# Kernel optimization log

Hardware: AMD Instinct MI355X
Metric: run time of the kernel (lower is better)

## Reference

```python
import jax, jax.numpy as jnp
import numpy as np

B, N_NODES, T_IN = 512, 32, 12
HID, HEADS, OUT_CH, DEG = 64, 8, 9, 8


def setup_inputs() -> dict:
    key = jax.random.key(0)
    ks = jax.random.split(key, 26)
    rn = lambda k, s, sc=0.1: (jax.random.normal(k, s, jnp.float32) * sc)
    E = B * N_NODES * DEG
    src = jax.random.randint(ks[0], (E,), 0, N_NODES, jnp.int32)
    dst = jax.random.randint(ks[1], (E,), 0, N_NODES, jnp.int32)
    off = jnp.repeat(jnp.arange(B, dtype=jnp.int32) * N_NODES, N_NODES * DEG)
    edge_index = jnp.stack([src + off, dst + off])  # block-diagonal batched graph
    x = jax.random.normal(ks[2], (B, N_NODES, T_IN), jnp.float32)
    return {
        "x": x,
        "edge_index": edge_index,
        # gat1: in=T_IN -> HEADS*HID, concat
        "W1": rn(ks[3], (T_IN, HEADS * HID)),
        "a_src1": rn(ks[4], (HEADS, HID)),
        "a_dst1": rn(ks[5], (HEADS, HID)),
        "b1": rn(ks[6], (HEADS * HID,), 0.01),
        # gat2: in=HEADS*HID -> HID, heads=1, mean (concat=False)
        "W2": rn(ks[7], (HEADS * HID, HID), 0.05),
        "a_src2": rn(ks[8], (1, HID)),
        "a_dst2": rn(ks[9], (1, HID)),
        "b2": rn(ks[10], (HID,), 0.01),
        "gamma": jnp.ones((HID,), jnp.float32),
        "beta": jnp.zeros((HID,), jnp.float32),
        # gru1: input_size=N_NODES(=32), hidden=HID
        "Wi1": rn(ks[11], (3 * HID, N_NODES)),
        "Wh1": rn(ks[12], (3 * HID, HID)),
        "bi1": rn(ks[13], (3 * HID,), 0.01),
        "bh1": rn(ks[14], (3 * HID,), 0.01),
        # gru2: input_size=HID, hidden=HID
        "Wi2": rn(ks[15], (3 * HID, HID)),
        "Wh2": rn(ks[16], (3 * HID, HID)),
        "bi2": rn(ks[17], (3 * HID,), 0.01),
        "bh2": rn(ks[18], (3 * HID,), 0.01),
        "Wf": rn(ks[19], (OUT_CH, HID)),
        "bf": rn(ks[20], (OUT_CH,), 0.01),
    }


def _gat_layer(x, src, dst, W, a_s, a_d, b, concat):
    # PyG GATConv (eval mode, self-loops already appended by caller)
    Nn = x.shape[0]
    heads, hc = a_s.shape
    h = (x @ W).reshape(Nn, heads, hc)                 # [N, H, C]
    es = jnp.sum(h * a_s, axis=-1)                     # [N, H]
    ed = jnp.sum(h * a_d, axis=-1)
    e = jax.nn.leaky_relu(es[src] + ed[dst], 0.2)      # [E, H]
    m = jax.ops.segment_max(e, dst, num_segments=Nn)
    p = jnp.exp(e - m[dst])
    s = jax.ops.segment_sum(p, dst, num_segments=Nn)
    alpha = p / (s[dst] + 1e-16)                       # per-dst softmax
    out = jax.ops.segment_sum(h[src] * alpha[:, :, None], dst, num_segments=Nn)
    out = out.reshape(Nn, heads * hc) if concat else out.mean(axis=1)
    return out + b


def _gru(x, Wi, Wh, bi, bh):
    # torch.nn.GRU (batch_first) single layer; x: [B, T, F]
    H = Wh.shape[1]
    xi = x @ Wi.T + bi                                 # [B, T, 3H]
    def step(h, xt):
        gh = h @ Wh.T + bh
        r = jax.nn.sigmoid(xt[:, :H] + gh[:, :H])
        z = jax.nn.sigmoid(xt[:, H:2 * H] + gh[:, H:2 * H])
        n = jnp.tanh(xt[:, 2 * H:] + r * gh[:, 2 * H:])
        hn = (1.0 - z) * n + z * h
        return hn, hn
    h0 = jnp.zeros((x.shape[0], H), x.dtype)
    _, ys = jax.lax.scan(step, h0, jnp.swapaxes(xi, 0, 1))
    return jnp.swapaxes(ys, 0, 1)


def reference(x, edge_index, W1, a_src1, a_dst1, b1, W2, a_src2, a_dst2, b2,
              gamma, beta, Wi1, Wh1, bi1, bh1, Wi2, Wh2, bi2, bh2, Wf, bf):
    Bsz, Nn_, T = x.shape
    Nn = Bsz * Nn_
    xf = x.reshape(Nn, T)                              # dropout is identity in eval
    sl = jnp.arange(Nn, dtype=edge_index.dtype)        # PyG add_self_loops=True
    src = jnp.concatenate([edge_index[0], sl])
    dst = jnp.concatenate([edge_index[1], sl])
    h = jax.nn.elu(_gat_layer(xf, src, dst, W1, a_src1, a_dst1, b1, True))
    h = jax.nn.elu(_gat_layer(h, src, dst, W2, a_src2, a_dst2, b2, False))
    mu = h.mean(-1, keepdims=True)
    var = ((h - mu) ** 2).mean(-1, keepdims=True)
    h = (h - mu) / jnp.sqrt(var + 1e-5) * gamma + beta
    seq = h.reshape(Bsz, Nn_, -1).transpose(0, 2, 1)   # [B, HID(seq), N_NODES(feat)]
    g = _gru(seq, Wi1, Wh1, bi1, bh1)
    g = _gru(g, Wi2, Wh2, bi2, bh2)
    return g[:, -1, :] @ Wf.T + bf                     # [B, OUT_CH]
```

## Files before the change

### kernel.cpp

```cpp
#include <hip/hip_runtime.h>
#include <hip/hip_bf16.h>
#include <stdint.h>

#define BATCH 512
#define NN 32
#define T_IN 12
#define HID 64
#define HEADS 8
#define OUT_CH 9
#define EPB (NN*8)
#define ETOT (EPB+NN)
#define F1 (HEADS*HID)

using u16 = unsigned short;
using u32 = unsigned int;
typedef _Float16 f16;
typedef _Float16 f16x2 __attribute__((ext_vector_type(2)));
typedef u32 v4u __attribute__((ext_vector_type(4)));
typedef float v4f __attribute__((ext_vector_type(4)));

__device__ __forceinline__ float bf2f(u16 u){ return __uint_as_float(((u32)u)<<16); }
__device__ __forceinline__ u16 f2bf(float f){
    u32 x = __float_as_uint(f);
    u32 r = (x + 0x7FFFu + ((x>>16)&1u))>>16;
    return (u16)r;
}
__device__ __forceinline__ u32 packf16(float a, float b){
    f16x2 p; p.x=(f16)a; p.y=(f16)b; return __builtin_bit_cast(u32,p);
}
__device__ __forceinline__ u16 f2h16(float a){ f16 h=(f16)a; return __builtin_bit_cast(u16,h); }
__device__ __forceinline__ float lof(u32 w){ return (float)__builtin_bit_cast(f16x2,w).x; }
__device__ __forceinline__ float hif(u32 w){ return (float)__builtin_bit_cast(f16x2,w).y; }
__device__ __forceinline__ float dot2(u32 a, u32 b, float c){
#if __has_builtin(__builtin_amdgcn_fdot2)
    return __builtin_amdgcn_fdot2(__builtin_bit_cast(f16x2,a), __builtin_bit_cast(f16x2,b), c, false);
#else
    return fmaf(lof(a),lof(b), fmaf(hif(a),hif(b), c));
#endif
}
__device__ __forceinline__ float elu1(float x){ return x > 0.f ? x : (__expf(x)-1.f); }
__device__ __forceinline__ float sigm(float x){ return 1.f/(1.f+__expf(-x)); }
__device__ __forceinline__ float tanh_(float x){ return 1.f - 2.f/(__expf(2.f*x)+1.f); }
__device__ __forceinline__ u32 fenc(float v){
    u32 b=__float_as_uint(v);
    return (b&0x80000000u) ? ~b : (b|0x80000000u);
}
__device__ __forceinline__ float fdec(u32 k){
    return __uint_as_float((k&0x80000000u) ? (k&0x7FFFFFFFu) : ~k);
}

#define DOT4(acc,A,W) do{ acc=dot2(A.x,W.x,acc); acc=dot2(A.y,W.y,acc); \
                          acc=dot2(A.z,W.z,acc); acc=dot2(A.w,W.w,acc); }while(0)

struct CvtDesc {
    const void* src[16];
    void*       dst[16];
    int         n[16];
};

__global__ __launch_bounds__(256) void k_setup(
    const u32* __restrict__ xw, CvtDesc d,
    const void* __restrict__ W2src, u16* __restrict__ W2i,
    const void* __restrict__ Wi1, const void* __restrict__ Wh1,
    const void* __restrict__ Wi2, const void* __restrict__ Wh2,
    u32* __restrict__ wpk, int* __restrict__ flag)
{
    __shared__ int cnt;
    if(threadIdx.x==0) cnt=0;
    __syncthreads();
    int c=0;
    for(int i=threadIdx.x;i<4096;i+=256){
        u32 w=xw[i];
        if(w & 0x7FFFFFFFu){
            u32 el=(w>>7)&0xFFu;
            if(el>=0x90u) c++;
        }
    }
    atomicAdd(&cnt,c);
    __syncthreads();
    const int f = (cnt>256) ? 1 : 0;
    if(blockIdx.x==0 && threadIdx.x==0) *flag=f;

    const int bk=blockIdx.x;
    if(bk<128){
        int seg=bk>>3, sub=bk&7;
        const void* s=d.src[seg];
        float* o=(float*)d.dst[seg];
        int n=d.n[seg];
        for(int i=sub*256+threadIdx.x;i<n;i+=2048)
            o[i] = f ? ((const float*)s)[i] : bf2f(((const u16*)s)[i]);
    } else if(bk<256){
        int i=(bk-128)*256+threadIdx.x;
        int k=i>>6, j=i&63;
        float v = f? ((const float*)W2src)[i] : bf2f(((const u16*)W2src)[i]);
        W2i[ (((size_t)(k>>3)*64 + j)<<3) + (k&7) ] = f2h16(v);
    } else {
        int w=(bk-256)*256+threadIdx.x;
        int m=w/6144;
        int rem=w-m*6144;
        int row=rem>>5, kw=rem&31;
        const void* s=(m==0)?Wi1:(m==1)?Wh1:(m==2)?Wi2:Wh2;
        int K=(m==0)?32:64;
        int k0=2*kw, k1=k0+1;
        float v0=0.f, v1=0.f;
        if(k0<K) v0 = f? ((const float*)s)[row*K+k0] : bf2f(((const u16*)s)[row*K+k0]);
        if(k1<K) v1 = f? ((const float*)s)[row*K+k1] : bf2f(((const u16*)s)[row*K+k1]);
        wpk[w]=packf16(v0,v1);
    }
}

__global__ __launch_bounds__(512,4) void k_fused(
    const float* __restrict__ x, const int* __restrict__ ei,
    const float* __restrict__ W1, const float* __restrict__ a_s, const float* __restrict__ a_d,
    const float* __restrict__ b1,
    const uint4* __restrict__ W2i, const float* __restrict__ a_s2, const float* __restrict__ a_d2,
    const float* __restrict__ b2, const float* __restrict__ gam, const float* __restrict__ bet,
    const u32* __restrict__ wpk,
    const float* __restrict__ bi1, const float* __restrict__ bh1,
    const float* __restrict__ bi2, const float* __restrict__ bh2,
    const float* __restrict__ Wf, const float* __restrict__ bfv,
    void* __restrict__ outp, const int* __restrict__ flag)
{
    const int b = blockIdx.x, t = threadIdx.x;

    __shared__ __align__(16) float s_x[NN][12];
    __shared__ __align__(16) u16 s_h[NN][520];
    __shared__ __align__(16) u32 s_aspk[HEADS*32], s_adpk[HEADS*32];
    __shared__ float s_es[NN][HEADS], s_ed[NN][HEADS];
    __shared__ unsigned char s_src[ETOT], s_dst[ETOT];
    __shared__ float s_al[HEADS][ETOT];
    __shared__ u32 s_mx[NN*HEADS];
    __shared__ float s_sm[NN*HEADS], s_inv[NN*HEADS];
    __shared__ int s_cnt[NN], s_off[NN], s_fil[NN];
    __shared__ short s_lst[ETOT];
    __shared__ float s_h2[NN][HID];
    __shared__ __align__(16) u32 s_x1[64*16];
    __shared__ __align__(16) u32 s_g1[2][32];
    __shared__ __align__(16) u32 s_g2[2][32];
    __shared__ float s_h2f[64];

    for(int i=t;i<NN*T_IN;i+=512) s_x[i/12][i%12] = x[b*NN*T_IN + i];
    if(t<256){
        s_aspk[t]=packf16(a_s[2*t],a_s[2*t+1]);
        s_adpk[t]=packf16(a_d[2*t],a_d[2*t+1]);
        s_mx[t]=0u; s_sm[t]=0.f;
    }
    if(t<EPB){
        s_src[t] = (unsigned char)(ei[b*EPB+t] - b*NN);
        s_dst[t] = (unsigned char)(ei[(size_t)BATCH*EPB + b*EPB+t] - b*NN);
    }
    if(t<NN){ s_src[EPB+t]=s_dst[EPB+t]=(unsigned char)t; s_cnt[t]=0; s_fil[t]=0; }
    v4f Wc0,Wc1,Wc2;
    Wc0.x=W1[0*F1+t]; Wc0.y=W1[1*F1+t]; Wc0.z=W1[2*F1+t]; Wc0.w=W1[3*F1+t];
    Wc1.x=W1[4*F1+t]; Wc1.y=W1[5*F1+t]; Wc1.z=W1[6*F1+t]; Wc1.w=W1[7*F1+t];
    Wc2.x=W1[8*F1+t]; Wc2.y=W1[9*F1+t]; Wc2.z=W1[10*F1+t]; Wc2.w=W1[11*F1+t];
    __syncthreads();

    for(int n=0;n<NN;n++){
        const float4* xp=(const float4*)s_x[n];
        float4 xa=xp[0], xb=xp[1], xc=xp[2];
        float A=0.f;
        A=fmaf(xa.x,Wc0.x,A); A=fmaf(xa.y,Wc0.y,A); A=fmaf(xa.z,Wc0.z,A); A=fmaf(xa.w,Wc0.w,A);
        A=fmaf(xb.x,Wc1.x,A); A=fmaf(xb.y,Wc1.y,A); A=fmaf(xb.z,Wc1.z,A); A=fmaf(xb.w,Wc1.w,A);
        A=fmaf(xc.x,Wc2.x,A); A=fmaf(xc.y,Wc2.y,A); A=fmaf(xc.z,Wc2.z,A); A=fmaf(xc.w,Wc2.w,A);
        s_h[n][t]=f2h16(A);
    }
    for(int e=t;e<ETOT;e+=512) atomicAdd(&s_cnt[s_dst[e]],1);
    __syncthreads();

    if(t<256){
        int n=t&31, hd=t>>5;
        const v4u* hp=(const v4u*)((const u16*)s_h[n] + hd*64);
        v4u h0=hp[0],h1=hp[1],h2=hp[2],h3=hp[3],h4=hp[4],h5=hp[5],h6=hp[6],h7=hp[7];
        const v4u* ap=(const v4u*)&s_aspk[hd*32];
        const v4u* dp=(const v4u*)&s_adpk[hd*32];
        float e1=0.f,e2=0.f;
        { v4u w=ap[0]; DOT4(e1,h0,w); w=ap[1]; DOT4(e1,h1,w); w=ap[2]; DOT4(e1,h2,w); w=ap[3]; DOT4(e1,h3,w);
          w=ap[4]; DOT4(e1,h4,w); w=ap[5]; DOT4(e1,h5,w); w=ap[6]; DOT4(e1,h6,w); w=ap[7]; DOT4(e1,h7,w); }
        { v4u w=dp[0]; DOT4(e2,h0,w); w=dp[1]; DOT4(e2,h1,w); w=dp[2]; DOT4(e2,h2,w); w=dp[3]; DOT4(e2,h3,w);
          w=dp[4]; DOT4(e2,h4,w); w=dp[5]; DOT4(e2,h5,w); w=dp[6]; DOT4(e2,h6,w); w=dp[7]; DOT4(e2,h7,w); }
        s_es[n][hd]=e1; s_ed[n][hd]=e2;
    }
    if(t==0){ int o=0; for(int i=0;i<NN;i++){ s_off[i]=o; o+=s_cnt[i]; } }
    __syncthreads();

    for(int e=t;e<ETOT;e+=512){
        int d=s_dst[e]; int p=atomicAdd(&s_fil[d],1); s_lst[s_off[d]+p]=(short)e;
    }
    for(int i=t;i<ETOT*HEADS;i+=512){
        int hd=i/ETOT, e=i-hd*ETOT;
        int sr=s_src[e], d=s_dst[e];
        float v = s_es[sr][hd]+s_ed[d][hd];
        v = v>0.f? v : 0.2f*v;
        s_al[hd][e]=v;
        atomicMax(&s_mx[d*8+hd], fenc(v));
    }
    __syncthreads();

    for(int i=t;i<ETOT*HEADS;i+=512){
        int hd=i/ETOT, e=i-hd*ETOT;
        int d=s_dst[e];
        float p=__expf(s_al[hd][e]-fdec(s_mx[d*8+hd]));
        s_al[hd][e]=p;
        atomicAdd(&s_sm[d*8+hd], p);
    }
    __syncthreads();
    if(t<256) s_inv[t]=1.f/(s_sm[t]+1e-16f);
    __syncthreads();

    u32 res[16];
    const int dA=t&31, hdA=(t>>5)&7, chA=t>>8;
    {
        int o=s_off[dA], cnt=s_cnt[dA];
        float inv=s_inv[dA*8+hdA];
        v4f a0=0,a1=0,a2=0,a3=0,a4=0,a5=0,a6=0,a7=0;
        for(int i=0;i<cnt;i++){
            int e=s_lst[o+i]; float av=s_al[hdA][e]; int sr=s_src[e];
            const v4u* hp=(const v4u*)((const u16*)s_h[sr] + hdA*64 + chA*32);
            v4u p0=hp[0],p1=hp[1],p2=hp[2],p3=hp[3];
            a0.x=fmaf(av,lof(p0.x),a0.x); a0.y=fmaf(av,hif(p0.x),a0.y);
            a0.z=fmaf(av,lof(p0.y),a0.z); a0.w=fmaf(av,hif(p0.y),a0.w);
            a1.x=fmaf(av,lof(p0.z),a1.x); a1.y=fmaf(av,hif(p0.z),a1.y);
            a1.z=fmaf(av,lof(p0.w),a1.z); a1.w=fmaf(av,hif(p0.w),a1.w);
            a2.x=fmaf(av,lof(p1.x),a2.x); a2.y=fmaf(av,hif(p1.x),a2.y);
            a2.z=fmaf(av,lof(p1.y),a2.z); a2.w=fmaf(av,hif(p1.y),a2.w);
            a3.x=fmaf(av,lof(p1.z),a3.x); a3.y=fmaf(av,hif(p1.z),a3.y);
            a3.z=fmaf(av,lof(p1.w),a3.z); a3.w=fmaf(av,hif(p1.w),a3.w);
            a4.x=fmaf(av,lof(p2.x),a4.x); a4.y=fmaf(av,hif(p2.x),a4.y);
            a4.z=fmaf(av,lof(p2.y),a4.z); a4.w=fmaf(av,hif(p2.y),a4.w);
            a5.x=fmaf(av,lof(p2.z),a5.x); a5.y=fmaf(av,hif(p2.z),a5.y);
            a5.z=fmaf(av,lof(p2.w),a5.z); a5.w=fmaf(av,hif(p2.w),a5.w);
            a6.x=fmaf(av,lof(p3.x),a6.x); a6.y=fmaf(av,hif(p3.x),a6.y);
            a6.z=fmaf(av,lof(p3.y),a6.z); a6.w=fmaf(av,hif(p3.y),a6.w);
            a7.x=fmaf(av,lof(p3.z),a7.x); a7.y=fmaf(av,hif(p3.z),a7.y);
            a7.z=fmaf(av,lof(p3.w),a7.z); a7.w=fmaf(av,hif(p3.w),a7.w);
        }
        const float* bp = b1 + hdA*64 + chA*32;
        res[0] = packf16(elu1(a0.x*inv+bp[0]),  elu1(a0.y*inv+bp[1]));
        res[1] = packf16(elu1(a0.z*inv+bp[2]),  elu1(a0.w*inv+bp[3]));
        res[2] = packf16(elu1(a1.x*inv+bp[4]),  elu1(a1.y*inv+bp[5]));
        res[3] = packf16(elu1(a1.z*inv+bp[6]),  elu1(a1.w*inv+bp[7]));
        res[4] = packf16(elu1(a2.x*inv+bp[8]),  elu1(a2.y*inv+bp[9]));
        res[5] = packf16(elu1(a2.z*inv+bp[10]), elu1(a2.w*inv+bp[11]));
        res[6] = packf16(elu1(a3.x*inv+bp[12]), elu1(a3.y*inv+bp[13]));
        res[7] = packf16(elu1(a3.z*inv+bp[14]), elu1(a3.w*inv+bp[15]));
        res[8] = packf16(elu1(a4.x*inv+bp[16]), elu1(a4.y*inv+bp[17]));
        res[9] = packf16(elu1(a4.z*inv+bp[18]), elu1(a4.w*inv+bp[19]));
        res[10]= packf16(elu1(a5.x*inv+bp[20]), elu1(a5.y*inv+bp[21]));
        res[11]= packf16(elu1(a5.z*inv+bp[22]), elu1(a5.w*inv+bp[23]));
        res[12]= packf16(elu1(a6.x*inv+bp[24]), elu1(a6.y*inv+bp[25]));
        res[13]= packf16(elu1(a6.z*inv+bp[26]), elu1(a6.w*inv+bp[27]));
        res[14]= packf16(elu1(a7.x*inv+bp[28]), elu1(a7.y*inv+bp[29]));
        res[15]= packf16(elu1(a7.z*inv+bp[30]), elu1(a7.w*inv+bp[31]));
    }
    __syncthreads();
    {
        u32* rw = ((u32*)s_h) + dA*260 + hdA*32 + chA*16;
        #pragma unroll
        for(int i=0;i<16;i++) rw[i]=res[i];
    }
    if(t<NN){ s_fil[t]=0; s_mx[t]=0u; s_sm[t]=0.f; }
    __syncthreads();

    {
        int n0=(t>>6)<<2, j=t&63;
        const u32* r0=((const u32*)s_h)+(n0+0)*260;
        const u32* r1=((const u32*)s_h)+(n0+1)*260;
        const u32* r2=((const u32*)s_h)+(n0+2)*260;
        const u32* r3=((const u32*)s_h)+(n0+3)*260;
        float a0=0,a1=0,a2=0,a3=0;
        for(int kb=0;kb<64;kb++){
            uint4 A0=*(const uint4*)&r0[kb*4];
            uint4 A1=*(const uint4*)&r1[kb*4];
            uint4 A2=*(const uint4*)&r2[kb*4];
            uint4 A3=*(const uint4*)&r3[kb*4];
            uint4 w0=W2i[kb*64+j];
            a0=dot2(A0.x,w0.x,a0); a0=dot2(A0.y,w0.y,a0); a0=dot2(A0.z,w0.z,a0); a0=dot2(A0.w,w0.w,a0);
            a1=dot2(A1.x,w0.x,a1); a1=dot2(A1.y,w0.y,a1); a1=dot2(A1.z,w0.z,a1); a1=dot2(A1.w,w0.w,a1);
            a2=dot2(A2.x,w0.x,a2); a2=dot2(A2.y,w0.y,a2); a2=dot2(A2.z,w0.z,a2); a2=dot2(A2.w,w0.w,a2);
            a3=dot2(A3.x,w0.x,a3); a3=dot2(A3.y,w0.y,a3); a3=dot2(A3.z,w0.z,a3); a3=dot2(A3.w,w0.w,a3);
        }
        s_h2[n0+0][j]=a0; s_h2[n0+1][j]=a1; s_h2[n0+2][j]=a2; s_h2[n0+3][j]=a3;
    }
    __syncthreads();

    if(t<256){
        int n=t>>3, g=t&7;
        float e1=0,e2=0;
        #pragma unroll
        for(int cc=0; cc<8; cc++){
            float hv = s_h2[n][g*8+cc];
            e1 += hv*a_s2[g*8+cc];
            e2 += hv*a_d2[g*8+cc];
        }
        #pragma unroll
        for(int m=1;m<8;m<<=1){ e1 += __shfl_xor(e1,m,64); e2 += __shfl_xor(e2,m,64); }
        if(g==0){ s_es[n][0]=e1; s_ed[n][0]=e2; }
    }
    __syncthreads();

    for(int e=t;e<ETOT;e+=512){
        int d=s_dst[e];
        float v = s_es[s_src[e]][0] + s_ed[d][0];
        v = v>0.f? v:0.2f*v;
        s_al[0][e]=v;
        atomicMax(&s_mx[d], fenc(v));
    }
    __syncthreads();

    for(int e=t;e<ETOT;e+=512){
        int d=s_dst[e];
        float p=__expf(s_al[0][e]-fdec(s_mx[d]));
        s_al[0][e]=p;
        atomicAdd(&s_sm[d], p);
    }
    __syncthreads();
    if(t<NN) s_inv[t]=1.f/(s_sm[t]+1e-16f);
    __syncthreads();

    if(t<256){
        int n=t>>3, g=t&7;
        v4f a0=0, a1=0;
        int o=s_off[n], cnt=s_cnt[n];
        float inv=s_inv[n];
        for(int i=0;i<cnt;i++){
            int e=s_lst[o+i]; float a=s_al[0][e]; int sr=s_src[e];
            const float4* hp=(const float4*)&s_h2[sr][g*8];
            float4 v0=hp[0], v1=hp[1];
            a0.x=fmaf(a,v0.x,a0.x); a0.y=fmaf(a,v0.y,a0.y); a0.z=fmaf(a,v0.z,a0.z); a0.w=fmaf(a,v0.w,a0.w);
            a1.x=fmaf(a,v1.x,a1.x); a1.y=fmaf(a,v1.y,a1.y); a1.z=fmaf(a,v1.z,a1.z); a1.w=fmaf(a,v1.w,a1.w);
        }
        const float* bp=b2+g*8;
        float v0=elu1(a0.x*inv+bp[0]), v1=elu1(a0.y*inv+bp[1]);
        float v2=elu1(a0.z*inv+bp[2]), v3=elu1(a0.w*inv+bp[3]);
        float v4=elu1(a1.x*inv+bp[4]), v5=elu1(a1.y*inv+bp[5]);
        float v6=elu1(a1.z*inv+bp[6]), v7=elu1(a1.w*inv+bp[7]);
        float sum=v0+v1+v2+v3+v4+v5+v6+v7;
        float sq=v0*v0+v1*v1+v2*v2+v3*v3+v4*v4+v5*v5+v6*v6+v7*v7;
        #pragma unroll
        for(int m=1;m<8;m<<=1){ sum+=__shfl_xor(sum,m,64); sq+=__shfl_xor(sq,m,64); }
        float mu = sum*(1.f/64.f);
        float var = sq*(1.f/64.f) - mu*mu;
        float rs = rsqrtf(var + 1e-5f);
        u16* xw=(u16*)s_x1;
        int c=g*8;
        xw[(c+0)*NN+n]=f2h16((v0-mu)*rs*gam[c+0]+bet[c+0]);
        xw[(c+1)*NN+n]=f2h16((v1-mu)*rs*gam[c+1]+bet[c+1]);
        xw[(c+2)*NN+n]=f2h16((v2-mu)*rs*gam[c+2]+bet[c+2]);
        xw[(c+3)*NN+n]=f2h16((v3-mu)*rs*gam[c+3]+bet[c+3]);
        xw[(c+4)*NN+n]=f2h16((v4-mu)*rs*gam[c+4]+bet[c+4]);
        xw[(c+5)*NN+n]=f2h16((v5-mu)*rs*gam[c+5]+bet[c+5]);
        xw[(c+6)*NN+n]=f2h16((v6-mu)*rs*gam[c+6]+bet[c+6]);
        xw[(c+7)*NN+n]=f2h16((v7-mu)*rs*gam[c+7]+bet[c+7]);
    }
    if(t<32){ s_g1[0][t]=0u; s_g1[1][t]=0u; s_g2[0][t]=0u; s_g2[1][t]=0u; }
    __syncthreads();

    {
        const int wave=t>>6, lane=t&63;
        const int layer=wave>>1;
        const int ublk=wave&1;
        const int uu=lane&31, s=lane>>5;
        const int u=ublk*32+uu;
        const bool gw = (t<256);

        u32 wiR[16],wiZ[16],wiN[16],whR[16],whZ[16],whN[16];
        float br=0.f,bz=0.f,bxn=0.f,bhn=0.f;
        if(gw){
            const u32* wiu = wpk + (size_t)(layer*2+0)*6144;
            const u32* whu = wpk + (size_t)(layer*2+1)*6144;
            if(layer==0){
                #pragma unroll
                for(int k=0;k<8;k++){
                    wiR[k]=wiu[u*32+s*8+k];
                    wiZ[k]=wiu[(64+u)*32+s*8+k];
                    wiN[k]=wiu[(128+u)*32+s*8+k];
                }
                #pragma unroll
                for(int k=0;k<16;k++){
                    whR[k]=whu[u*32+s*16+k];
                    whZ[k]=whu[(64+u)*32+s*16+k];
                    whN[k]=whu[(128+u)*32+s*16+k];
                }
            } else {
                #pragma unroll
                for(int k=0;k<16;k++){
                    wiR[k]=wiu[u*32+s*16+k];
                    wiZ[k]=wiu[(64+u)*32+s*16+k];
                    wiN[k]=wiu[(128+u)*32+s*16+k];
                    whR[k]=whu[u*32+s*16+k];
                    whZ[k]=whu[(64+u)*32+s*16+k];
                    whN[k]=whu[(128+u)*32+s*16+k];
                }
            }
            const float* bi = layer? bi2:bi1;
            const float* bh = layer? bh2:bh1;
            br=bi[u]+bh[u]; bz=bi[64+u]+bh[64+u]; bxn=bi[128+u]; bhn=bh[128+u];
        }
        float h=0.f;

        for(int it=0; it<=64; ++it){
            const int pb=(it-1)&1, cb=it&1;
            bool act=false;
            float pr=0.f,pz=0.f,pxn=0.f,phn=0.f;
            if(gw){
                if(layer==0){
                    act=(it<64);
                    if(act){
                        const u32* xp=&s_x1[it*16+s*8];
                        const u32* hp=&s_g1[pb][s*16];
                        #pragma unroll
                        for(int k=0;k<8;k++){ u32 xv=xp[k]; pr=dot2(xv,wiR[k],pr); pz=dot2(xv,wiZ[k],pz); pxn=dot2(xv,wiN[k],pxn); }
                        #pragma unroll
                        for(int k=0;k<16;k++){ u32 hv=hp[k]; pr=dot2(hv,whR[k],pr); pz=dot2(hv,whZ[k],pz); phn=dot2(hv,whN[k],phn); }
                    }
                } else {
                    act=(it>=1);
                    if(act){
                        const u32* xp=&s_g1[pb][s*16];
                        const u32* hp=&s_g2[pb][s*16];
                        #pragma unroll
                        for(int k=0;k<16;k++){
                            u32 xv=xp[k], hv=hp[k];
                            pr=dot2(xv,wiR[k],pr); pz=dot2(xv,wiZ[k],pz); pxn=dot2(xv,wiN[k],pxn);
                            pr=dot2(hv,whR[k],pr); pz=dot2(hv,whZ[k],pz); phn=dot2(hv,whN[k],phn);
                        }
                    }
                }
            }
            if(act){
                pr  += __shfl_xor(pr ,32,64);
                pz  += __shfl_xor(pz ,32,64);
                pxn += __shfl_xor(pxn,32,64);
                phn += __shfl_xor(phn,32,64);
                float r=sigm(pr+br), z=sigm(pz+bz);
                float n=tanh_(pxn+bxn + r*(phn+bhn));
                h=(1.f-z)*n + z*h;
                if(s==0){
                    u16 hv=f2h16(h);
                    if(layer==0) ((u16*)s_g1[cb])[u]=hv;
                    else { ((u16*)s_g2[cb])[u]=hv; if(it==64) s_h2f[u]=h; }
                }
            }
            __syncthreads();
        }
    }

    if(t<OUT_CH){
        float acc=bfv[t];
        const float4* wp=(const float4*)(Wf + t*64);
        const float4* hp=(const float4*)s_h2f;
        #pragma unroll
        for(int k=0;k<16;k++){
            float4 w=wp[k], v=hp[k];
            acc += w.x*v.x + w.y*v.y + w.z*v.z + w.w*v.w;
        }
        if(*flag) ((float*)outp)[b*OUT_CH+t]=acc;
        else      ((u16*)outp)[b*OUT_CH+t]=f2bf(acc);
    }
}

extern "C" void kernel_launch(void* const* d_in, const int* in_sizes, int n_in,
                              void* d_out, int out_size, void* d_ws, size_t ws_size,
                              hipStream_t stream)
{
    char* ws=(char*)d_ws;
    int* flag = (int*)ws;
    float* cf = (float*)(ws + 256);
    float* c_x   = cf; cf+=196608;
    float* c_W1  = cf; cf+=6144;
    float* c_as1 = cf; cf+=512;
    float* c_ad1 = cf; cf+=512;
    float* c_b1  = cf; cf+=512;
    float* c_as2 = cf; cf+=64;
    float* c_ad2 = cf; cf+=64;
    float* c_b2  = cf; cf+=64;
    float* c_gam = cf; cf+=64;
    float* c_bet = cf; cf+=64;
    float* c_bi1 = cf; cf+=192;
    float* c_bh1 = cf; cf+=192;
    float* c_bi2 = cf; cf+=192;
    float* c_bh2 = cf; cf+=192;
    float* c_Wf  = cf; cf+=576;
    float* c_bf  = cf; cf+=9;
    uintptr_t p = ((uintptr_t)cf + 255) & ~(uintptr_t)255;
    u16* c_W2i = (u16*)p;
    p = (p + 32768*2 + 255) & ~(uintptr_t)255;
    u32* wpk = (u32*)p;

    const int* ei = (const int*)d_in[1];

    CvtDesc d;
    const int srcIdx[16] = {0,2,3,4,5,7,8,9,10,11,14,15,18,19,20,21};
    void* dsts[16] = {c_x,c_W1,c_as1,c_ad1,c_b1,c_as2,c_ad2,c_b2,c_gam,c_bet,
                      c_bi1,c_bh1,c_bi2,c_bh2,c_Wf,c_bf};
    const int ns[16] = {196608,6144,512,512,512,64,64,64,64,64,
                        192,192,192,192,576,9};
    for(int i=0;i<16;i++){ d.src[i]=d_in[srcIdx[i]]; d.dst[i]=dsts[i]; d.n[i]=ns[i]; }

    k_setup <<<dim3(352),dim3(256),0,stream>>>((const u32*)d_in[0], d,
                                               d_in[6], c_W2i,
                                               d_in[12], d_in[13], d_in[16], d_in[17],
                                               wpk, flag);
    k_fused <<<dim3(BATCH),dim3(512),0,stream>>>(
        c_x, ei, c_W1, c_as1, c_ad1, c_b1,
        (const uint4*)c_W2i, c_as2, c_ad2, c_b2, c_gam, c_bet,
        wpk, c_bi1, c_bh1, c_bi2, c_bh2,
        c_Wf, c_bf, d_out, flag);
}
```

Measured before the change: 254.6 us.

## Split fused GAT+GRU kernel into separate GAT and GRU kernels

The single fused kernel is split in two. The first runs both GAT layers and the layer norm, then writes the normalized features to a global workspace in fp32. A separate 256-thread kernel loads those features, packs them to fp16 in LDS, and runs the two-layer GRU recurrence plus the final linear. This drops the 256 idle threads that sat through the 65 serial GRU steps and frees the GAT kernel of the GRU weight registers, and inline-asm pins keep the GRU weights resident in registers. The cost is an extra launch and a global round trip for the intermediate features.

```diff
diff --git a/kernel.cpp b/kernel.cpp
--- a/kernel.cpp
+++ b/kernel.cpp
@@ -51,6 +51,8 @@
 
 #define DOT4(acc,A,W) do{ acc=dot2(A.x,W.x,acc); acc=dot2(A.y,W.y,acc); \
                           acc=dot2(A.z,W.z,acc); acc=dot2(A.w,W.w,acc); }while(0)
+
+#define PIN(v) asm("" : "+v"(v))
 
 struct CvtDesc {
     const void* src[16];
@@ -109,17 +111,13 @@
     }
 }
 
-__global__ __launch_bounds__(512,4) void k_fused(
+__global__ __launch_bounds__(512,4) void k_ab(
     const float* __restrict__ x, const int* __restrict__ ei,
     const float* __restrict__ W1, const float* __restrict__ a_s, const float* __restrict__ a_d,
     const float* __restrict__ b1,
     const uint4* __restrict__ W2i, const float* __restrict__ a_s2, const float* __restrict__ a_d2,
     const float* __restrict__ b2, const float* __restrict__ gam, const float* __restrict__ bet,
-    const u32* __restrict__ wpk,
-    const float* __restrict__ bi1, const float* __restrict__ bh1,
-    const float* __restrict__ bi2, const float* __restrict__ bh2,
-    const float* __restrict__ Wf, const float* __restrict__ bfv,
-    void* __restrict__ outp, const int* __restrict__ flag)
+    float* __restrict__ hlng)
 {
     const int b = blockIdx.x, t = threadIdx.x;
 
@@ -134,10 +132,6 @@
     __shared__ int s_cnt[NN], s_off[NN], s_fil[NN];
     __shared__ short s_lst[ETOT];
     __shared__ float s_h2[NN][HID];
-    __shared__ __align__(16) u32 s_x1[64*16];
-    __shared__ __align__(16) u32 s_g1[2][32];
-    __shared__ __align__(16) u32 s_g2[2][32];
-    __shared__ float s_h2f[64];
 
     for(int i=t;i<NN*T_IN;i+=512) s_x[i/12][i%12] = x[b*NN*T_IN + i];
     if(t<256){
@@ -342,108 +336,126 @@
         float mu = sum*(1.f/64.f);
         float var = sq*(1.f/64.f) - mu*mu;
         float rs = rsqrtf(var + 1e-5f);
-        u16* xw=(u16*)s_x1;
+        float* op = hlng + (size_t)b*HID*NN;
         int c=g*8;
-        xw[(c+0)*NN+n]=f2h16((v0-mu)*rs*gam[c+0]+bet[c+0]);
-        xw[(c+1)*NN+n]=f2h16((v1-mu)*rs*gam[c+1]+bet[c+1]);
-        xw[(c+2)*NN+n]=f2h16((v2-mu)*rs*gam[c+2]+bet[c+2]);
-        xw[(c+3)*NN+n]=f2h16((v3-mu)*rs*gam[c+3]+bet[c+3]);
-        xw[(c+4)*NN+n]=f2h16((v4-mu)*rs*gam[c+4]+bet[c+4]);
-        xw[(c+5)*NN+n]=f2h16((v5-mu)*rs*gam[c+5]+bet[c+5]);
-        xw[(c+6)*NN+n]=f2h16((v6-mu)*rs*gam[c+6]+bet[c+6]);
-        xw[(c+7)*NN+n]=f2h16((v7-mu)*rs*gam[c+7]+bet[c+7]);
-    }
-    if(t<32){ s_g1[0][t]=0u; s_g1[1][t]=0u; s_g2[0][t]=0u; s_g2[1][t]=0u; }
-    __syncthreads();
-
-    {
-        const int wave=t>>6, lane=t&63;
-        const int layer=wave>>1;
-        const int ublk=wave&1;
-        const int uu=lane&31, s=lane>>5;
-        const int u=ublk*32+uu;
-        const bool gw = (t<256);
-
-        u32 wiR[16],wiZ[16],wiN[16],whR[16],whZ[16],whN[16];
-        float br=0.f,bz=0.f,bxn=0.f,bhn=0.f;
-        if(gw){
-            const u32* wiu = wpk + (size_t)(layer*2+0)*6144;
-            const u32* whu = wpk + (size_t)(layer*2+1)*6144;
-            if(layer==0){
+        op[(c+0)*NN+n]=(v0-mu)*rs*gam[c+0]+bet[c+0];
+        op[(c+1)*NN+n]=(v1-mu)*rs*gam[c+1]+bet[c+1];
+        op[(c+2)*NN+n]=(v2-mu)*rs*gam[c+2]+bet[c+2];
+        op[(c+3)*NN+n]=(v3-mu)*rs*gam[c+3]+bet[c+3];
+        op[(c+4)*NN+n]=(v4-mu)*rs*gam[c+4]+bet[c+4];
+        op[(c+5)*NN+n]=(v5-mu)*rs*gam[c+5]+bet[c+5];
+        op[(c+6)*NN+n]=(v6-mu)*rs*gam[c+6]+bet[c+6];
+        op[(c+7)*NN+n]=(v7-mu)*rs*gam[c+7]+bet[c+7];
+    }
+}
+
+__global__ __launch_bounds__(256,2) void k_gruf(
+    const float* __restrict__ hlng, const u32* __restrict__ wpk,
+    const float* __restrict__ bi1, const float* __restrict__ bh1,
+    const float* __restrict__ bi2, const float* __restrict__ bh2,
+    const float* __restrict__ Wf, const float* __restrict__ bfv,
+    void* __restrict__ outp, const int* __restrict__ flag)
+{
+    const int b=blockIdx.x, t=threadIdx.x;
+    const int wave=t>>6, lane=t&63;
+    const int layer=wave>>1;
+    const int ublk=wave&1;
+    const int uu=lane&31, s=lane>>5;
+    const int u=ublk*32+uu;
+
+    __shared__ __align__(16) u32 s_x1[64*16];
+    __shared__ __align__(16) u32 s_h1[2][32];
+    __shared__ __align__(16) u32 s_h2[2][32];
+    __shared__ float s_h2f[64];
+
+    { const float2* g=(const float2*)(hlng + (size_t)b*2048);
+      for(int w=t;w<1024;w+=256){ float2 v=g[w]; s_x1[w]=packf16(v.x,v.y); } }
+    if(t<32){ s_h1[0][t]=0u; s_h1[1][t]=0u; s_h2[0][t]=0u; s_h2[1][t]=0u; }
+
+    u32 wiR[16],wiZ[16],wiN[16],whR[16],whZ[16],whN[16];
+    const u32* wiu = wpk + (size_t)(layer*2+0)*6144;
+    const u32* whu = wpk + (size_t)(layer*2+1)*6144;
+    if(layer==0){
+        #pragma unroll
+        for(int k=0;k<8;k++){
+            wiR[k]=wiu[u*32+s*8+k];
+            wiZ[k]=wiu[(64+u)*32+s*8+k];
+            wiN[k]=wiu[(128+u)*32+s*8+k];
+        }
+        #pragma unroll
+        for(int k=0;k<8;k++){ PIN(wiR[k]); PIN(wiZ[k]); PIN(wiN[k]); }
+        #pragma unroll
+        for(int k=0;k<16;k++){
+            whR[k]=whu[u*32+s*16+k];
+            whZ[k]=whu[(64+u)*32+s*16+k];
+            whN[k]=whu[(128+u)*32+s*16+k];
+        }
+        #pragma unroll
+        for(int k=0;k<16;k++){ PIN(whR[k]); PIN(whZ[k]); PIN(whN[k]); }
+    } else {
+        #pragma unroll
+        for(int k=0;k<16;k++){
+            wiR[k]=wiu[u*32+s*16+k];
+            wiZ[k]=wiu[(64+u)*32+s*16+k];
+            wiN[k]=wiu[(128+u)*32+s*16+k];
+            whR[k]=whu[u*32+s*16+k];
+            whZ[k]=whu[(64+u)*32+s*16+k];
+            whN[k]=whu[(128+u)*32+s*16+k];
+        }
+        #pragma unroll
+        for(int k=0;k<16;k++){
+            PIN(wiR[k]); PIN(wiZ[k]); PIN(wiN[k]);
+            PIN(whR[k]); PIN(whZ[k]); PIN(whN[k]);
+        }
+    }
+    const float* bi = layer? bi2:bi1;
+    const float* bh = layer? bh2:bh1;
+    float br=bi[u]+bh[u], bz=bi[64+u]+bh[64+u], bxn=bi[128+u], bhn=bh[128+u];
+    float h=0.f;
+    __syncthreads();
+
+    for(int it=0; it<=64; ++it){
+        const int pb=(it-1)&1, cb=it&1;
+        bool act;
+        float pr=0.f,pz=0.f,pxn=0.f,phn=0.f;
+        if(layer==0){
+            act=(it<64);
+            if(act){
+                const u32* xp=&s_x1[it*16+s*8];
+                const u32* hp=&s_h1[pb][s*16];
                 #pragma unroll
-                for(int k=0;k<8;k++){
-                    wiR[k]=wiu[u*32+s*8+k];
-                    wiZ[k]=wiu[(64+u)*32+s*8+k];
-                    wiN[k]=wiu[(128+u)*32+s*8+k];
-                }
+                for(int k=0;k<8;k++){ u32 xv=xp[k]; pr=dot2(xv,wiR[k],pr); pz=dot2(xv,wiZ[k],pz); pxn=dot2(xv,wiN[k],pxn); }
+                #pragma unroll
+                for(int k=0;k<16;k++){ u32 hv=hp[k]; pr=dot2(hv,whR[k],pr); pz=dot2(hv,whZ[k],pz); phn=dot2(hv,whN[k],phn); }
+            }
+        } else {
+            act=(it>=1);
+            if(act){
+                const u32* xp=&s_h1[pb][s*16];
+                const u32* hp=&s_h2[pb][s*16];
                 #pragma unroll
                 for(int k=0;k<16;k++){
-                    whR[k]=whu[u*32+s*16+k];
-                    whZ[k]=whu[(64+u)*32+s*16+k];
-                    whN[k]=whu[(128+u)*32+s*16+k];
-                }
-            } else {
-                #pragma unroll
-                for(int k=0;k<16;k++){
-                    wiR[k]=wiu[u*32+s*16+k];
-                    wiZ[k]=wiu[(64+u)*32+s*16+k];
-                    wiN[k]=wiu[(128+u)*32+s*16+k];
-                    whR[k]=whu[u*32+s*16+k];
-                    whZ[k]=whu[(64+u)*32+s*16+k];
-                    whN[k]=whu[(128+u)*32+s*16+k];
+                    u32 xv=xp[k], hv=hp[k];
+                    pr=dot2(xv,wiR[k],pr); pz=dot2(xv,wiZ[k],pz); pxn=dot2(xv,wiN[k],pxn);
+                    pr=dot2(hv,whR[k],pr); pz=dot2(hv,whZ[k],pz); phn=dot2(hv,whN[k],phn);
                 }
             }
-            const float* bi = layer? bi2:bi1;
-            const float* bh = layer? bh2:bh1;
-            br=bi[u]+bh[u]; bz=bi[64+u]+bh[64+u]; bxn=bi[128+u]; bhn=bh[128+u];
-        }
-        float h=0.f;
-
-        for(int it=0; it<=64; ++it){
-            const int pb=(it-1)&1, cb=it&1;
-            bool act=false;
-            float pr=0.f,pz=0.f,pxn=0.f,phn=0.f;
-            if(gw){
-                if(layer==0){
-                    act=(it<64);
-                    if(act){
-                        const u32* xp=&s_x1[it*16+s*8];
-                        const u32* hp=&s_g1[pb][s*16];
-                        #pragma unroll
-                        for(int k=0;k<8;k++){ u32 xv=xp[k]; pr=dot2(xv,wiR[k],pr); pz=dot2(xv,wiZ[k],pz); pxn=dot2(xv,wiN[k],pxn); }
-                        #pragma unroll
-                        for(int k=0;k<16;k++){ u32 hv=hp[k]; pr=dot2(hv,whR[k],pr); pz=dot2(hv,whZ[k],pz); phn=dot2(hv,whN[k],phn); }
-                    }
-                } else {
-                    act=(it>=1);
-                    if(act){
-                        const u32* xp=&s_g1[pb][s*16];
-                        const u32* hp=&s_g2[pb][s*16];
-                        #pragma unroll
-                        for(int k=0;k<16;k++){
-                            u32 xv=xp[k], hv=hp[k];
-                            pr=dot2(xv,wiR[k],pr); pz=dot2(xv,wiZ[k],pz); pxn=dot2(xv,wiN[k],pxn);
-                            pr=dot2(hv,whR[k],pr); pz=dot2(hv,whZ[k],pz); phn=dot2(hv,whN[k],phn);
-                        }
-                    }
-                }
+        }
+        if(act){
+            pr  += __shfl_xor(pr ,32,64);
+            pz  += __shfl_xor(pz ,32,64);
+            pxn += __shfl_xor(pxn,32,64);
+            phn += __shfl_xor(phn,32,64);
+            float r=sigm(pr+br), z=sigm(pz+bz);
+            float n=tanh_(pxn+bxn + r*(phn+bhn));
+            h=(1.f-z)*n + z*h;
+            if(s==0){
+                u16 hv=f2h16(h);
+                if(layer==0) ((u16*)s_h1[cb])[u]=hv;
+                else { ((u16*)s_h2[cb])[u]=hv; if(it==64) s_h2f[u]=h; }
             }
-            if(act){
-                pr  += __shfl_xor(pr ,32,64);
-                pz  += __shfl_xor(pz ,32,64);
-                pxn += __shfl_xor(pxn,32,64);
-                phn += __shfl_xor(phn,32,64);
-                float r=sigm(pr+br), z=sigm(pz+bz);
-                float n=tanh_(pxn+bxn + r*(phn+bhn));
-                h=(1.f-z)*n + z*h;
-                if(s==0){
-                    u16 hv=f2h16(h);
-                    if(layer==0) ((u16*)s_g1[cb])[u]=hv;
-                    else { ((u16*)s_g2[cb])[u]=hv; if(it==64) s_h2f[u]=h; }
-                }
-            }
-            __syncthreads();
-        }
+        }
+        __syncthreads();
     }
 
     if(t<OUT_CH){
@@ -487,6 +499,8 @@
     u16* c_W2i = (u16*)p;
     p = (p + 32768*2 + 255) & ~(uintptr_t)255;
     u32* wpk = (u32*)p;
+    p = (p + 24576*4 + 255) & ~(uintptr_t)255;
+    float* hlng = (float*)p;
 
     const int* ei = (const int*)d_in[1];
 
@@ -502,9 +516,9 @@
                                                d_in[6], c_W2i,
                                                d_in[12], d_in[13], d_in[16], d_in[17],
                                                wpk, flag);
-    k_fused <<<dim3(BATCH),dim3(512),0,stream>>>(
+    k_ab    <<<dim3(BATCH),dim3(512),0,stream>>>(
         c_x, ei, c_W1, c_as1, c_ad1, c_b1,
-        (const uint4*)c_W2i, c_as2, c_ad2, c_b2, c_gam, c_bet,
-        wpk, c_bi1, c_bh1, c_bi2, c_bh2,
-        c_Wf, c_bf, d_out, flag);
-}
+        (const uint4*)c_W2i, c_as2, c_ad2, c_b2, c_gam, c_bet, hlng);
+    k_gruf  <<<dim3(BATCH),dim3(256),0,stream>>>(hlng, wpk, c_bi1,c_bh1,c_bi2,c_bh2,
+                                                 c_Wf, c_bf, d_out, flag);
+}
```

After: 216.9 us, median of 2. 14.8% less time.
